# Kernel tuning notes

Hardware: AMD Instinct MI355X
Metric: run time of the kernel (lower is better)

The kernel has to match this reference:

```python
import jax, jax.numpy as jnp
import numpy as np

N = 50000       # node_num
E_RND = 1600000 # random edges (avg degree 32)
IN = 256        # in_dim
OUT = 128       # out_dim
NB = 10000      # queried nodes batch
SLOPE = 0.1     # leaky_relu slope_ratio


def setup_inputs() -> dict:
    key = jax.random.key(0)
    k = jax.random.split(key, 6)
    feats = jax.random.normal(k[0], (N, IN), dtype=jnp.float32)
    W = jax.random.normal(k[1], (OUT, IN), dtype=jnp.float32) * 0.05
    b = jax.random.normal(k[2], (OUT,), dtype=jnp.float32) * 0.05
    a = jax.random.normal(k[3], (2 * OUT,), dtype=jnp.float32) * 0.05
    rnd = jax.random.randint(k[4], (E_RND, 2), 0, N)
    loops = jnp.stack([jnp.arange(N), jnp.arange(N)], axis=1)  # self-loops, as in torch code
    edges = jnp.concatenate([rnd, loops], axis=0).astype(jnp.int32)  # [E,2] = (dst, src)
    node_idx = jax.random.randint(k[5], (NB,), 0, N).astype(jnp.int32)
    return dict(feats=feats, W=W, b=b, a=a, edges=edges, node_idx=node_idx)


def reference(feats, W, b, a, edges, node_idx):
    n = feats.shape[0]
    emb = feats @ W.T + b                      # [N, OUT]  (out_linear_layer)
    out_dim = emb.shape[1]
    # concat(emb[dst], emb[src]) @ a  ==  (emb @ a1)[dst] + (emb @ a2)[src]
    s_dst = emb @ a[:out_dim]                  # [N]
    s_src = emb @ a[out_dim:]                  # [N]
    dst, src = edges[:, 0], edges[:, 1]
    score = jnp.exp(jax.nn.leaky_relu(s_dst[dst] + s_src[src], negative_slope=SLOPE))  # [E]
    # sparse.mm(matrix, emb) and sparse.mm(matrix, ones) as segment sums over dst
    num = jax.ops.segment_sum(score[:, None] * emb[src], dst, num_segments=n)  # [N, OUT]
    den = jax.ops.segment_sum(score, dst, num_segments=n)                       # [N]
    out = num / den[:, None]
    return out[node_idx]
```

## Files before the change

### kernel.cpp

```cpp
#include <hip/hip_runtime.h>

#define IN_DIM 256
#define OUT_DIM 128
#define SLOPE 0.1f
#define CAP 128

typedef short bf16x8 __attribute__((ext_vector_type(8)));
typedef float f32x4  __attribute__((ext_vector_type(4)));

__device__ __forceinline__ unsigned short f2bf(float f) {
    unsigned u = __builtin_bit_cast(unsigned, f);
    return (unsigned short)((u + 0x7FFFu + ((u >> 16) & 1u)) >> 16);
}

__global__ __launch_bounds__(256) void gemm_mfma_kernel(
    const float* __restrict__ feats, const float* __restrict__ W,
    const float* __restrict__ bias, const float* __restrict__ a,
    unsigned short* __restrict__ emb_bf, float* __restrict__ s_dst,
    float* __restrict__ s_src, int* __restrict__ needed,
    int* __restrict__ cur, int n)
{
    __shared__ __align__(16) unsigned short A_s[128 * 128];
    __shared__ __align__(16) unsigned short W_s[128 * 128];
    __shared__ float sd_l[2][128];
    __shared__ float ss_l[2][128];

    const int t    = threadIdx.x;
    const int lane = t & 63;
    const int wid  = t >> 6;
    const int wr   = wid >> 1;
    const int wc   = wid & 1;
    const int row0 = blockIdx.x * 128;

    if (t < 128) {
        const int ci = row0 + t;
        if (ci < n) { needed[ci] = 0; cur[ci] = 0; }
    }

    const f32x4 z4 = {0.f, 0.f, 0.f, 0.f};
    f32x4 acc[4][4];
    #pragma unroll
    for (int mi = 0; mi < 4; ++mi)
        #pragma unroll
        for (int ni = 0; ni < 4; ++ni) acc[mi][ni] = z4;

    for (int ph = 0; ph < 2; ++ph) {
        const int k0 = ph * 128;
        if (ph) __syncthreads();

        #pragma unroll
        for (int i = 0; i < 8; ++i) {
            const int g = i * 256 + t;
            const int r = g >> 4;
            const int c = g & 15;
            const int gr = row0 + r;
            float4 v0 = make_float4(0.f,0.f,0.f,0.f), v1 = v0;
            if (gr < n) {
                v0 = *(const float4*)&feats[(size_t)gr * IN_DIM + k0 + c * 8];
                v1 = *(const float4*)&feats[(size_t)gr * IN_DIM + k0 + c * 8 + 4];
            }
            bf16x8 pk;
            pk[0]=(short)f2bf(v0.x); pk[1]=(short)f2bf(v0.y);
            pk[2]=(short)f2bf(v0.z); pk[3]=(short)f2bf(v0.w);
            pk[4]=(short)f2bf(v1.x); pk[5]=(short)f2bf(v1.y);
            pk[6]=(short)f2bf(v1.z); pk[7]=(short)f2bf(v1.w);
            const int off = (r * 128 + c * 8) ^ ((r & 7) << 3);
            *(bf16x8*)&A_s[off] = pk;
        }
        #pragma unroll
        for (int i = 0; i < 8; ++i) {
            const int g = i * 256 + t;
            const int r = g >> 4;
            const int c = g & 15;
            const float4 v0 = *(const float4*)&W[(size_t)r * IN_DIM + k0 + c * 8];
            const float4 v1 = *(const float4*)&W[(size_t)r * IN_DIM + k0 + c * 8 + 4];
            bf16x8 pk;
            pk[0]=(short)f2bf(v0.x); pk[1]=(short)f2bf(v0.y);
            pk[2]=(short)f2bf(v0.z); pk[3]=(short)f2bf(v0.w);
            pk[4]=(short)f2bf(v1.x); pk[5]=(short)f2bf(v1.y);
            pk[6]=(short)f2bf(v1.z); pk[7]=(short)f2bf(v1.w);
            const int off = (r * 128 + c * 8) ^ ((r & 7) << 3);
            *(bf16x8*)&W_s[off] = pk;
        }
        __syncthreads();

        #pragma unroll
        for (int ks = 0; ks < 4; ++ks) {
            const int kf = ks * 32 + (lane >> 4) * 8;
            bf16x8 af[4], wf[4];
            #pragma unroll
            for (int mi = 0; mi < 4; ++mi) {
                const int row = wr * 64 + mi * 16 + (lane & 15);
                const int off = (row * 128 + kf) ^ ((row & 7) << 3);
                af[mi] = *(const bf16x8*)&A_s[off];
            }
            #pragma unroll
            for (int ni = 0; ni < 4; ++ni) {
                const int col = wc * 64 + ni * 16 + (lane & 15);
                const int off = (col * 128 + kf) ^ ((col & 7) << 3);
                wf[ni] = *(const bf16x8*)&W_s[off];
            }
            #pragma unroll
            for (int mi = 0; mi < 4; ++mi)
                #pragma unroll
                for (int ni = 0; ni < 4; ++ni)
                    acc[mi][ni] = __builtin_amdgcn_mfma_f32_16x16x32_bf16(
                        af[mi], wf[ni], acc[mi][ni], 0, 0, 0);
        }
    }

    float bcol[4], avd[4], avs[4];
    #pragma unroll
    for (int ni = 0; ni < 4; ++ni) {
        const int col = wc * 64 + ni * 16 + (lane & 15);
        bcol[ni] = bias[col];
        avd[ni]  = a[col];
        avs[ni]  = a[OUT_DIM + col];
    }

    #pragma unroll
    for (int mi = 0; mi < 4; ++mi) {
        #pragma unroll
        for (int j = 0; j < 4; ++j) {
            const int rib = wr * 64 + mi * 16 + (lane >> 4) * 4 + j;
            const int row = row0 + rib;
            float pd = 0.f, ps = 0.f;
            if (row < n) {
                #pragma unroll
                for (int ni = 0; ni < 4; ++ni) {
                    const float v = acc[mi][ni][j] + bcol[ni];
                    emb_bf[(size_t)row * OUT_DIM + wc * 64 + ni * 16 + (lane & 15)] = f2bf(v);
                    pd = fmaf(v, avd[ni], pd);
                    ps = fmaf(v, avs[ni], ps);
                }
            }
            pd += __shfl_xor(pd, 1); ps += __shfl_xor(ps, 1);
            pd += __shfl_xor(pd, 2); ps += __shfl_xor(ps, 2);
            pd += __shfl_xor(pd, 4); ps += __shfl_xor(ps, 4);
            pd += __shfl_xor(pd, 8); ps += __shfl_xor(ps, 8);
            if ((lane & 15) == 0) { sd_l[wc][rib] = pd; ss_l[wc][rib] = ps; }
        }
    }
    __syncthreads();
    if (t < 128) {
        const int row = row0 + t;
        if (row < n) {
            s_dst[row] = sd_l[0][t] + sd_l[1][t];
            s_src[row] = ss_l[0][t] + ss_l[1][t];
        }
    }
}

__global__ void flag_kernel(const int* __restrict__ node_idx,
                            int* __restrict__ needed, int nb)
{
    const int i = blockIdx.x * blockDim.x + threadIdx.x;
    if (i < nb) needed[node_idx[i]] = 1;
}

__global__ __launch_bounds__(256) void scatter_kernel(
    const int* __restrict__ edges, const int* __restrict__ needed,
    int* __restrict__ cur, const float* __restrict__ s_dst,
    const float* __restrict__ s_src, int2* __restrict__ ew, int E)
{
    const int e = blockIdx.x * blockDim.x + threadIdx.x;
    if (e >= E) return;
    const int2 ed = reinterpret_cast<const int2*>(edges)[e];
    if (needed[ed.x]) {
        const float x = s_dst[ed.x] + s_src[ed.y];
        const float w = __expf(x >= 0.f ? x : SLOPE * x);
        const int p = atomicAdd(&cur[ed.x], 1);
        if (p < CAP)
            ew[(size_t)ed.x * CAP + p] = make_int2(ed.y, __float_as_int(w));
    }
}

__global__ __launch_bounds__(256) void agg_out_kernel(
    const int* __restrict__ node_idx, const int* __restrict__ cur,
    const int2* __restrict__ ew, const unsigned short* __restrict__ emb_bf,
    float* __restrict__ out, int nb)
{
    const int w    = (int)((blockIdx.x * blockDim.x + threadIdx.x) >> 6);
    const int lane = threadIdx.x & 63;
    if (w >= nb) return;

    const int dst = node_idx[w];
    int m = cur[dst];
    if (m > CAP) m = CAP;
    const int2* __restrict__ bucket = ew + (size_t)dst * CAP;

    float accx = 0.f, accy = 0.f, den = 0.f;

    for (int base = 0; base < m; base += 64) {
        const int rem = min(64, m - base);
        int   src = 0;
        float wt  = 0.f;
        if (lane < rem) {
            const int2 q = bucket[base + lane];
            src = q.x;
            wt  = __int_as_float(q.y);
        }
        int i = 0;
        for (; i + 4 <= rem; i += 4) {
            const int   s0 = __shfl(src, i),     s1 = __shfl(src, i + 1);
            const int   s2 = __shfl(src, i + 2), s3 = __shfl(src, i + 3);
            const float w0 = __shfl(wt, i),      w1 = __shfl(wt, i + 1);
            const float w2 = __shfl(wt, i + 2),  w3 = __shfl(wt, i + 3);
            const unsigned b0 = *(const unsigned*)&emb_bf[(size_t)s0 * OUT_DIM + 2 * lane];
            const unsigned b1 = *(const unsigned*)&emb_bf[(size_t)s1 * OUT_DIM + 2 * lane];
            const unsigned b2 = *(const unsigned*)&emb_bf[(size_t)s2 * OUT_DIM + 2 * lane];
            const unsigned b3 = *(const unsigned*)&emb_bf[(size_t)s3 * OUT_DIM + 2 * lane];
            den += (w0 + w1) + (w2 + w3);
            accx = fmaf(w0, __int_as_float((int)(b0 << 16)), accx);
            accy = fmaf(w0, __int_as_float((int)(b0 & 0xFFFF0000u)), accy);
            accx = fmaf(w1, __int_as_float((int)(b1 << 16)), accx);
            accy = fmaf(w1, __int_as_float((int)(b1 & 0xFFFF0000u)), accy);
            accx = fmaf(w2, __int_as_float((int)(b2 << 16)), accx);
            accy = fmaf(w2, __int_as_float((int)(b2 & 0xFFFF0000u)), accy);
            accx = fmaf(w3, __int_as_float((int)(b3 << 16)), accx);
            accy = fmaf(w3, __int_as_float((int)(b3 & 0xFFFF0000u)), accy);
        }
        for (; i < rem; ++i) {
            const int   s0 = __shfl(src, i);
            const float w0 = __shfl(wt, i);
            const unsigned b0 = *(const unsigned*)&emb_bf[(size_t)s0 * OUT_DIM + 2 * lane];
            den += w0;
            accx = fmaf(w0, __int_as_float((int)(b0 << 16)), accx);
            accy = fmaf(w0, __int_as_float((int)(b0 & 0xFFFF0000u)), accy);
        }
    }

    const float inv = 1.0f / den;
    float2 o; o.x = accx * inv; o.y = accy * inv;
    *reinterpret_cast<float2*>(&out[(size_t)w * OUT_DIM + 2 * lane]) = o;
}

extern "C" void kernel_launch(void* const* d_in, const int* in_sizes, int n_in,
                              void* d_out, int out_size, void* d_ws, size_t ws_size,
                              hipStream_t stream)
{
    const float* feats    = (const float*)d_in[0];
    const float* W        = (const float*)d_in[1];
    const float* bias     = (const float*)d_in[2];
    const float* a        = (const float*)d_in[3];
    const int*   edges    = (const int*)d_in[4];
    const int*   node_idx = (const int*)d_in[5];
    float*       out      = (float*)d_out;

    const int n  = in_sizes[0] / IN_DIM;
    const int E  = in_sizes[4] / 2;
    const int nb = in_sizes[5];

    char* ws = (char*)d_ws;
    unsigned short* emb_bf = (unsigned short*)ws;
    ws += (size_t)n * OUT_DIM * sizeof(unsigned short);
    float* s_dst = (float*)ws;  ws += (size_t)(n + 4) * sizeof(float);
    float* s_src = (float*)ws;  ws += (size_t)(n + 4) * sizeof(float);
    int*   needed= (int*)ws;    ws += (size_t)(n + 4) * sizeof(int);
    int*   cur   = (int*)ws;    ws += (size_t)(n + 4) * sizeof(int);
    int2*  ew    = (int2*)ws;   ws += (size_t)n * CAP * sizeof(int2);

    gemm_mfma_kernel<<<(n + 127) / 128, 256, 0, stream>>>(
        feats, W, bias, a, emb_bf, s_dst, s_src, needed, cur, n);
    flag_kernel     <<<(nb + 255) / 256, 256, 0, stream>>>(node_idx, needed, nb);
    scatter_kernel  <<<(E + 255) / 256, 256, 0, stream>>>(edges, needed, cur, s_dst, s_src, ew, E);
    agg_out_kernel  <<<(nb + 3) / 4, 256, 0, stream>>>(node_idx, cur, ew, emb_bf, out, nb);
}
```

Baseline: 63.52 us.

## Shrink GEMM row tile, stage emb stores through LDS, drop needed-node filter

The GEMM now handles 64 rows per block instead of 128, which halves the accumulator registers and launches twice as many blocks. The bf16 embedding is first written into padded shared memory and then stored to global memory as coalesced 16-byte vectors. The flag kernel and the `needed` array are removed, so the scatter pass now scores and buckets every edge, not only edges into queried nodes. That saves one launch and one memset-like write, but it raises scatter work, atomics and bucket writes roughly fivefold.

```diff
diff --git a/kernel.cpp b/kernel.cpp
--- a/kernel.cpp
+++ b/kernel.cpp
@@ -17,30 +17,29 @@
     const float* __restrict__ feats, const float* __restrict__ W,
     const float* __restrict__ bias, const float* __restrict__ a,
     unsigned short* __restrict__ emb_bf, float* __restrict__ s_dst,
-    float* __restrict__ s_src, int* __restrict__ needed,
-    int* __restrict__ cur, int n)
-{
-    __shared__ __align__(16) unsigned short A_s[128 * 128];
+    float* __restrict__ s_src, int* __restrict__ cur, int n)
+{
+    __shared__ __align__(16) unsigned short A_s[64 * 136];
     __shared__ __align__(16) unsigned short W_s[128 * 128];
-    __shared__ float sd_l[2][128];
-    __shared__ float ss_l[2][128];
+    __shared__ float sd_l[2][64];
+    __shared__ float ss_l[2][64];
 
     const int t    = threadIdx.x;
     const int lane = t & 63;
     const int wid  = t >> 6;
     const int wr   = wid >> 1;
     const int wc   = wid & 1;
-    const int row0 = blockIdx.x * 128;
-
-    if (t < 128) {
+    const int row0 = blockIdx.x * 64;
+
+    if (t < 64) {
         const int ci = row0 + t;
-        if (ci < n) { needed[ci] = 0; cur[ci] = 0; }
+        if (ci < n) cur[ci] = 0;
     }
 
     const f32x4 z4 = {0.f, 0.f, 0.f, 0.f};
-    f32x4 acc[4][4];
-    #pragma unroll
-    for (int mi = 0; mi < 4; ++mi)
+    f32x4 acc[2][4];
+    #pragma unroll
+    for (int mi = 0; mi < 2; ++mi)
         #pragma unroll
         for (int ni = 0; ni < 4; ++ni) acc[mi][ni] = z4;
 
@@ -49,7 +48,7 @@
         if (ph) __syncthreads();
 
         #pragma unroll
-        for (int i = 0; i < 8; ++i) {
+        for (int i = 0; i < 4; ++i) {
             const int g = i * 256 + t;
             const int r = g >> 4;
             const int c = g & 15;
@@ -87,10 +86,10 @@
         #pragma unroll
         for (int ks = 0; ks < 4; ++ks) {
             const int kf = ks * 32 + (lane >> 4) * 8;
-            bf16x8 af[4], wf[4];
-            #pragma unroll
-            for (int mi = 0; mi < 4; ++mi) {
-                const int row = wr * 64 + mi * 16 + (lane & 15);
+            bf16x8 af[2], wf[4];
+            #pragma unroll
+            for (int mi = 0; mi < 2; ++mi) {
+                const int row = wr * 32 + mi * 16 + (lane & 15);
                 const int off = (row * 128 + kf) ^ ((row & 7) << 3);
                 af[mi] = *(const bf16x8*)&A_s[off];
             }
@@ -101,7 +100,7 @@
                 wf[ni] = *(const bf16x8*)&W_s[off];
             }
             #pragma unroll
-            for (int mi = 0; mi < 4; ++mi)
+            for (int mi = 0; mi < 2; ++mi)
                 #pragma unroll
                 for (int ni = 0; ni < 4; ++ni)
                     acc[mi][ni] = __builtin_amdgcn_mfma_f32_16x16x32_bf16(
@@ -118,21 +117,20 @@
         avs[ni]  = a[OUT_DIM + col];
     }
 
-    #pragma unroll
-    for (int mi = 0; mi < 4; ++mi) {
+    __syncthreads();
+
+    #pragma unroll
+    for (int mi = 0; mi < 2; ++mi) {
         #pragma unroll
         for (int j = 0; j < 4; ++j) {
-            const int rib = wr * 64 + mi * 16 + (lane >> 4) * 4 + j;
-            const int row = row0 + rib;
+            const int rib = wr * 32 + mi * 16 + (lane >> 4) * 4 + j;
             float pd = 0.f, ps = 0.f;
-            if (row < n) {
-                #pragma unroll
-                for (int ni = 0; ni < 4; ++ni) {
-                    const float v = acc[mi][ni][j] + bcol[ni];
-                    emb_bf[(size_t)row * OUT_DIM + wc * 64 + ni * 16 + (lane & 15)] = f2bf(v);
-                    pd = fmaf(v, avd[ni], pd);
-                    ps = fmaf(v, avs[ni], ps);
-                }
+            #pragma unroll
+            for (int ni = 0; ni < 4; ++ni) {
+                const float v = acc[mi][ni][j] + bcol[ni];
+                A_s[rib * 136 + wc * 64 + ni * 16 + (lane & 15)] = f2bf(v);
+                pd = fmaf(v, avd[ni], pd);
+                ps = fmaf(v, avs[ni], ps);
             }
             pd += __shfl_xor(pd, 1); ps += __shfl_xor(ps, 1);
             pd += __shfl_xor(pd, 2); ps += __shfl_xor(ps, 2);
@@ -142,7 +140,19 @@
         }
     }
     __syncthreads();
-    if (t < 128) {
+
+    #pragma unroll
+    for (int i = 0; i < 4; ++i) {
+        const int g = i * 256 + t;
+        const int r = g >> 4;
+        const int c8 = g & 15;
+        const int gr = row0 + r;
+        if (gr < n) {
+            const bf16x8 v = *(const bf16x8*)&A_s[r * 136 + c8 * 8];
+            *(bf16x8*)&emb_bf[(size_t)gr * OUT_DIM + c8 * 8] = v;
+        }
+    }
+    if (t < 64) {
         const int row = row0 + t;
         if (row < n) {
             s_dst[row] = sd_l[0][t] + sd_l[1][t];
@@ -151,28 +161,19 @@
     }
 }
 
-__global__ void flag_kernel(const int* __restrict__ node_idx,
-                            int* __restrict__ needed, int nb)
-{
-    const int i = blockIdx.x * blockDim.x + threadIdx.x;
-    if (i < nb) needed[node_idx[i]] = 1;
-}
-
 __global__ __launch_bounds__(256) void scatter_kernel(
-    const int* __restrict__ edges, const int* __restrict__ needed,
-    int* __restrict__ cur, const float* __restrict__ s_dst,
-    const float* __restrict__ s_src, int2* __restrict__ ew, int E)
+    const int* __restrict__ edges, int* __restrict__ cur,
+    const float* __restrict__ s_dst, const float* __restrict__ s_src,
+    int2* __restrict__ ew, int E)
 {
     const int e = blockIdx.x * blockDim.x + threadIdx.x;
     if (e >= E) return;
     const int2 ed = reinterpret_cast<const int2*>(edges)[e];
-    if (needed[ed.x]) {
-        const float x = s_dst[ed.x] + s_src[ed.y];
-        const float w = __expf(x >= 0.f ? x : SLOPE * x);
-        const int p = atomicAdd(&cur[ed.x], 1);
-        if (p < CAP)
-            ew[(size_t)ed.x * CAP + p] = make_int2(ed.y, __float_as_int(w));
-    }
+    const float x = s_dst[ed.x] + s_src[ed.y];
+    const float w = __expf(x >= 0.f ? x : SLOPE * x);
+    const int p = atomicAdd(&cur[ed.x], 1);
+    if (p < CAP)
+        ew[(size_t)ed.x * CAP + p] = make_int2(ed.y, __float_as_int(w));
 }
 
 __global__ __launch_bounds__(256) void agg_out_kernel(
@@ -256,13 +257,11 @@
     ws += (size_t)n * OUT_DIM * sizeof(unsigned short);
     float* s_dst = (float*)ws;  ws += (size_t)(n + 4) * sizeof(float);
     float* s_src = (float*)ws;  ws += (size_t)(n + 4) * sizeof(float);
-    int*   needed= (int*)ws;    ws += (size_t)(n + 4) * sizeof(int);
     int*   cur   = (int*)ws;    ws += (size_t)(n + 4) * sizeof(int);
     int2*  ew    = (int2*)ws;   ws += (size_t)n * CAP * sizeof(int2);
 
-    gemm_mfma_kernel<<<(n + 127) / 128, 256, 0, stream>>>(
-        feats, W, bias, a, emb_bf, s_dst, s_src, needed, cur, n);
-    flag_kernel     <<<(nb + 255) / 256, 256, 0, stream>>>(node_idx, needed, nb);
-    scatter_kernel  <<<(E + 255) / 256, 256, 0, stream>>>(edges, needed, cur, s_dst, s_src, ew, E);
+    gemm_mfma_kernel<<<(n + 63) / 64, 256, 0, stream>>>(
+        feats, W, bias, a, emb_bf, s_dst, s_src, cur, n);
+    scatter_kernel  <<<(E + 255) / 256, 256, 0, stream>>>(edges, cur, s_dst, s_src, ew, E);
     agg_out_kernel  <<<(nb + 3) / 4, 256, 0, stream>>>(node_idx, cur, ew, emb_bf, out, nb);
 }
```

Result: slower. 130.5 us (+105.4%).

## Pre-convert inputs to bf16 and stage GEMM tiles via direct global-to-LDS loads

Applied to the files above, without the earlier changes.

Adds a separate conversion kernel that turns feats and W into bf16 buffers in the workspace. The GEMM then fills its LDS tiles with global_load_lds 16-byte direct copies, with the XOR swizzle applied on the source side, instead of loading fp32, converting in registers and writing to LDS. The goal is to cut register and VALU work and LDS write traffic in the GEMM staging. The cost is an extra full pass over feats (read fp32, write bf16, read bf16 again) plus one more kernel launch. The padded rows of the bf16 buffer are never written by the conversion kernel, so the last tile reads uninitialized data for rows beyond n.

```diff
diff --git a/kernel.cpp b/kernel.cpp
--- a/kernel.cpp
+++ b/kernel.cpp
@@ -7,14 +7,39 @@
 
 typedef short bf16x8 __attribute__((ext_vector_type(8)));
 typedef float f32x4  __attribute__((ext_vector_type(4)));
+typedef unsigned short ushort4v __attribute__((ext_vector_type(4)));
 
 __device__ __forceinline__ unsigned short f2bf(float f) {
     unsigned u = __builtin_bit_cast(unsigned, f);
     return (unsigned short)((u + 0x7FFFu + ((u >> 16) & 1u)) >> 16);
 }
 
+__device__ __forceinline__ void gld_lds16(const void* g, void* l) {
+    __builtin_amdgcn_global_load_lds(
+        (const __attribute__((address_space(1))) void*)g,
+        (__attribute__((address_space(3))) void*)l, 16, 0, 0);
+}
+
+__global__ __launch_bounds__(256) void cvt_kernel(
+    const float* __restrict__ feats, const float* __restrict__ W,
+    unsigned short* __restrict__ fb, unsigned short* __restrict__ wb,
+    int nf4, int nw4)
+{
+    const int stride = gridDim.x * blockDim.x;
+    const int total = nf4 + nw4;
+    for (int i = blockIdx.x * blockDim.x + threadIdx.x; i < total; i += stride) {
+        float4 v;
+        if (i < nf4) v = reinterpret_cast<const float4*>(feats)[i];
+        else         v = reinterpret_cast<const float4*>(W)[i - nf4];
+        ushort4v o;
+        o[0] = f2bf(v.x); o[1] = f2bf(v.y); o[2] = f2bf(v.z); o[3] = f2bf(v.w);
+        if (i < nf4) *reinterpret_cast<ushort4v*>(&fb[4 * (size_t)i]) = o;
+        else         *reinterpret_cast<ushort4v*>(&wb[4 * (size_t)(i - nf4)]) = o;
+    }
+}
+
 __global__ __launch_bounds__(256) void gemm_mfma_kernel(
-    const float* __restrict__ feats, const float* __restrict__ W,
+    const unsigned short* __restrict__ fb, const unsigned short* __restrict__ wb,
     const float* __restrict__ bias, const float* __restrict__ a,
     unsigned short* __restrict__ emb_bf, float* __restrict__ s_dst,
     float* __restrict__ s_src, int* __restrict__ needed,
@@ -37,6 +62,9 @@
         if (ci < n) { needed[ci] = 0; cur[ci] = 0; }
     }
 
+    const int rlo = lane >> 4;
+    const int cA  = lane & 15;
+
     const f32x4 z4 = {0.f, 0.f, 0.f, 0.f};
     f32x4 acc[4][4];
     #pragma unroll
@@ -49,38 +77,14 @@
         if (ph) __syncthreads();
 
         #pragma unroll
-        for (int i = 0; i < 8; ++i) {
-            const int g = i * 256 + t;
-            const int r = g >> 4;
-            const int c = g & 15;
-            const int gr = row0 + r;
-            float4 v0 = make_float4(0.f,0.f,0.f,0.f), v1 = v0;
-            if (gr < n) {
-                v0 = *(const float4*)&feats[(size_t)gr * IN_DIM + k0 + c * 8];
-                v1 = *(const float4*)&feats[(size_t)gr * IN_DIM + k0 + c * 8 + 4];
-            }
-            bf16x8 pk;
-            pk[0]=(short)f2bf(v0.x); pk[1]=(short)f2bf(v0.y);
-            pk[2]=(short)f2bf(v0.z); pk[3]=(short)f2bf(v0.w);
-            pk[4]=(short)f2bf(v1.x); pk[5]=(short)f2bf(v1.y);
-            pk[6]=(short)f2bf(v1.z); pk[7]=(short)f2bf(v1.w);
-            const int off = (r * 128 + c * 8) ^ ((r & 7) << 3);
-            *(bf16x8*)&A_s[off] = pk;
-        }
-        #pragma unroll
-        for (int i = 0; i < 8; ++i) {
-            const int g = i * 256 + t;
-            const int r = g >> 4;
-            const int c = g & 15;
-            const float4 v0 = *(const float4*)&W[(size_t)r * IN_DIM + k0 + c * 8];
-            const float4 v1 = *(const float4*)&W[(size_t)r * IN_DIM + k0 + c * 8 + 4];
-            bf16x8 pk;
-            pk[0]=(short)f2bf(v0.x); pk[1]=(short)f2bf(v0.y);
-            pk[2]=(short)f2bf(v0.z); pk[3]=(short)f2bf(v0.w);
-            pk[4]=(short)f2bf(v1.x); pk[5]=(short)f2bf(v1.y);
-            pk[6]=(short)f2bf(v1.z); pk[7]=(short)f2bf(v1.w);
-            const int off = (r * 128 + c * 8) ^ ((r & 7) << 3);
-            *(bf16x8*)&W_s[off] = pk;
+        for (int j = 0; j < 8; ++j) {
+            const int slot = wid * 8 + j;
+            const int r    = slot * 4 + rlo;
+            const int ch   = cA ^ (r & 7);
+            gld_lds16(fb + (size_t)(row0 + r) * IN_DIM + k0 + (ch << 3),
+                      &A_s[slot * 512]);
+            gld_lds16(wb + (size_t)r * IN_DIM + k0 + (ch << 3),
+                      &W_s[slot * 512]);
         }
         __syncthreads();
 
@@ -250,18 +254,27 @@
     const int n  = in_sizes[0] / IN_DIM;
     const int E  = in_sizes[4] / 2;
     const int nb = in_sizes[5];
+    const int npad = ((n + 127) / 128) * 128;
 
     char* ws = (char*)d_ws;
     unsigned short* emb_bf = (unsigned short*)ws;
     ws += (size_t)n * OUT_DIM * sizeof(unsigned short);
+    unsigned short* fb = (unsigned short*)ws;
+    ws += (size_t)npad * IN_DIM * sizeof(unsigned short);
+    unsigned short* wb = (unsigned short*)ws;
+    ws += (size_t)OUT_DIM * IN_DIM * sizeof(unsigned short);
     float* s_dst = (float*)ws;  ws += (size_t)(n + 4) * sizeof(float);
     float* s_src = (float*)ws;  ws += (size_t)(n + 4) * sizeof(float);
     int*   needed= (int*)ws;    ws += (size_t)(n + 4) * sizeof(int);
     int*   cur   = (int*)ws;    ws += (size_t)(n + 4) * sizeof(int);
     int2*  ew    = (int2*)ws;   ws += (size_t)n * CAP * sizeof(int2);
 
-    gemm_mfma_kernel<<<(n + 127) / 128, 256, 0, stream>>>(
-        feats, W, bias, a, emb_bf, s_dst, s_src, needed, cur, n);
+    const int nf4 = n * IN_DIM / 4;
+    const int nw4 = OUT_DIM * IN_DIM / 4;
+
+    cvt_kernel      <<<2048, 256, 0, stream>>>(feats, W, fb, wb, nf4, nw4);
+    gemm_mfma_kernel<<<npad / 128, 256, 0, stream>>>(
+        fb, wb, bias, a, emb_bf, s_dst, s_src, needed, cur, n);
     flag_kernel     <<<(nb + 255) / 256, 256, 0, stream>>>(node_idx, needed, nb);
     scatter_kernel  <<<(E + 255) / 256, 256, 0, stream>>>(edges, needed, cur, s_dst, s_src, ew, E);
     agg_out_kernel  <<<(nb + 3) / 4, 256, 0, stream>>>(node_idx, cur, ew, emb_bf, out, nb);
```

Measured after the change: 69.12 us. +8.8%, slower.

## Restructure GEMM as persistent per-wave row chunks with full W in LDS

Applied to the files above, without the earlier changes.

The GEMM kernel now runs a fixed grid of 512 blocks. Each block loads the whole 128x256 weight matrix into LDS once as bf16. Each wave then loops over 16-row chunks, reading feature rows straight from global memory into MFMA registers, and computes all 128 output columns itself. This removes the A-tile LDS staging, the block-level syncs between K phases and the cross-wave shared reduction of attention scores. In exchange, every block re-reads the full W, the 64KB LDS footprint limits occupancy, and the fixed grid size assumes enough threads to zero the needed/cur arrays.

```diff
diff --git a/kernel.cpp b/kernel.cpp
--- a/kernel.cpp
+++ b/kernel.cpp
@@ -11,6 +11,13 @@
 __device__ __forceinline__ unsigned short f2bf(float f) {
     unsigned u = __builtin_bit_cast(unsigned, f);
     return (unsigned short)((u + 0x7FFFu + ((u >> 16) & 1u)) >> 16);
+}
+
+__device__ __forceinline__ void pack8(const float4& v0, const float4& v1, bf16x8& pk) {
+    pk[0]=(short)f2bf(v0.x); pk[1]=(short)f2bf(v0.y);
+    pk[2]=(short)f2bf(v0.z); pk[3]=(short)f2bf(v0.w);
+    pk[4]=(short)f2bf(v1.x); pk[5]=(short)f2bf(v1.y);
+    pk[6]=(short)f2bf(v1.z); pk[7]=(short)f2bf(v1.w);
 }
 
 __global__ __launch_bounds__(256) void gemm_mfma_kernel(
@@ -18,135 +25,99 @@
     const float* __restrict__ bias, const float* __restrict__ a,
     unsigned short* __restrict__ emb_bf, float* __restrict__ s_dst,
     float* __restrict__ s_src, int* __restrict__ needed,
-    int* __restrict__ cur, int n)
-{
-    __shared__ __align__(16) unsigned short A_s[128 * 128];
-    __shared__ __align__(16) unsigned short W_s[128 * 128];
-    __shared__ float sd_l[2][128];
-    __shared__ float ss_l[2][128];
+    int* __restrict__ cur, int n, int nchunks)
+{
+    __shared__ __align__(16) unsigned short W_s[128 * 256];
 
     const int t    = threadIdx.x;
     const int lane = t & 63;
     const int wid  = t >> 6;
-    const int wr   = wid >> 1;
-    const int wc   = wid & 1;
-    const int row0 = blockIdx.x * 128;
-
-    if (t < 128) {
-        const int ci = row0 + t;
-        if (ci < n) { needed[ci] = 0; cur[ci] = 0; }
-    }
-
-    const f32x4 z4 = {0.f, 0.f, 0.f, 0.f};
-    f32x4 acc[4][4];
+
+    const int gi = blockIdx.x * 256 + t;
+    if (gi < n) { needed[gi] = 0; cur[gi] = 0; }
+
     #pragma unroll
-    for (int mi = 0; mi < 4; ++mi)
-        #pragma unroll
-        for (int ni = 0; ni < 4; ++ni) acc[mi][ni] = z4;
-
-    for (int ph = 0; ph < 2; ++ph) {
-        const int k0 = ph * 128;
-        if (ph) __syncthreads();
-
-        #pragma unroll
-        for (int i = 0; i < 8; ++i) {
-            const int g = i * 256 + t;
-            const int r = g >> 4;
-            const int c = g & 15;
-            const int gr = row0 + r;
-            float4 v0 = make_float4(0.f,0.f,0.f,0.f), v1 = v0;
-            if (gr < n) {
-                v0 = *(const float4*)&feats[(size_t)gr * IN_DIM + k0 + c * 8];
-                v1 = *(const float4*)&feats[(size_t)gr * IN_DIM + k0 + c * 8 + 4];
-            }
-            bf16x8 pk;
-            pk[0]=(short)f2bf(v0.x); pk[1]=(short)f2bf(v0.y);
-            pk[2]=(short)f2bf(v0.z); pk[3]=(short)f2bf(v0.w);
-            pk[4]=(short)f2bf(v1.x); pk[5]=(short)f2bf(v1.y);
-            pk[6]=(short)f2bf(v1.z); pk[7]=(short)f2bf(v1.w);
-            const int off = (r * 128 + c * 8) ^ ((r & 7) << 3);
-            *(bf16x8*)&A_s[off] = pk;
-        }
-        #pragma unroll
-        for (int i = 0; i < 8; ++i) {
-            const int g = i * 256 + t;
-            const int r = g >> 4;
-            const int c = g & 15;
-            const float4 v0 = *(const float4*)&W[(size_t)r * IN_DIM + k0 + c * 8];
-            const float4 v1 = *(const float4*)&W[(size_t)r * IN_DIM + k0 + c * 8 + 4];
-            bf16x8 pk;
-            pk[0]=(short)f2bf(v0.x); pk[1]=(short)f2bf(v0.y);
-            pk[2]=(short)f2bf(v0.z); pk[3]=(short)f2bf(v0.w);
-            pk[4]=(short)f2bf(v1.x); pk[5]=(short)f2bf(v1.y);
-            pk[6]=(short)f2bf(v1.z); pk[7]=(short)f2bf(v1.w);
-            const int off = (r * 128 + c * 8) ^ ((r & 7) << 3);
-            *(bf16x8*)&W_s[off] = pk;
-        }
-        __syncthreads();
-
-        #pragma unroll
-        for (int ks = 0; ks < 4; ++ks) {
-            const int kf = ks * 32 + (lane >> 4) * 8;
-            bf16x8 af[4], wf[4];
-            #pragma unroll
-            for (int mi = 0; mi < 4; ++mi) {
-                const int row = wr * 64 + mi * 16 + (lane & 15);
-                const int off = (row * 128 + kf) ^ ((row & 7) << 3);
-                af[mi] = *(const bf16x8*)&A_s[off];
-            }
-            #pragma unroll
-            for (int ni = 0; ni < 4; ++ni) {
-                const int col = wc * 64 + ni * 16 + (lane & 15);
-                const int off = (col * 128 + kf) ^ ((col & 7) << 3);
-                wf[ni] = *(const bf16x8*)&W_s[off];
-            }
-            #pragma unroll
-            for (int mi = 0; mi < 4; ++mi)
-                #pragma unroll
-                for (int ni = 0; ni < 4; ++ni)
-                    acc[mi][ni] = __builtin_amdgcn_mfma_f32_16x16x32_bf16(
-                        af[mi], wf[ni], acc[mi][ni], 0, 0, 0);
-        }
-    }
-
-    float bcol[4], avd[4], avs[4];
+    for (int i = 0; i < 16; ++i) {
+        const int g = i * 256 + t;
+        const int r = g >> 5;
+        const int c = g & 31;
+        const float* p = &W[(size_t)r * IN_DIM + c * 8];
+        const float4 v0 = *(const float4*)p;
+        const float4 v1 = *(const float4*)(p + 4);
+        bf16x8 pk; pack8(v0, v1, pk);
+        *(bf16x8*)&W_s[r * 256 + ((c ^ (r & 7)) << 3)] = pk;
+    }
+    __syncthreads();
+
+    const int rl = lane & 15;
+    const int kq = lane >> 4;
+    float bcol[8], avd[8], avs[8];
     #pragma unroll
-    for (int ni = 0; ni < 4; ++ni) {
-        const int col = wc * 64 + ni * 16 + (lane & 15);
+    for (int ni = 0; ni < 8; ++ni) {
+        const int col = ni * 16 + rl;
         bcol[ni] = bias[col];
         avd[ni]  = a[col];
         avs[ni]  = a[OUT_DIM + col];
     }
 
-    #pragma unroll
-    for (int mi = 0; mi < 4; ++mi) {
+    const int wstart  = blockIdx.x * 4 + wid;
+    const int wstride = gridDim.x * 4;
+
+    for (int chunk = wstart; chunk < nchunks; chunk += wstride) {
+        const int row0 = chunk * 16;
+        const int arow = row0 + rl;
+        const int lrow = arow < n ? arow : n - 1;
+        const float* prow = &feats[(size_t)lrow * IN_DIM + kq * 8];
+
+        bf16x8 af[8];
+        #pragma unroll
+        for (int ks = 0; ks < 8; ++ks) {
+            const float4 v0 = *(const float4*)(prow + ks * 32);
+            const float4 v1 = *(const float4*)(prow + ks * 32 + 4);
+            pack8(v0, v1, af[ks]);
+        }
+
+        f32x4 acc[8];
+        #pragma unroll
+        for (int ni = 0; ni < 8; ++ni) acc[ni] = {0.f, 0.f, 0.f, 0.f};
+
+        #pragma unroll
+        for (int ks = 0; ks < 8; ++ks) {
+            const int kf = ks * 32 + kq * 8;
+            #pragma unroll
+            for (int ni = 0; ni < 8; ++ni) {
+                const int col = ni * 16 + rl;
+                const int off = (col * 256 + kf) ^ ((col & 7) << 3);
+                const bf16x8 wf = *(const bf16x8*)&W_s[off];
+                acc[ni] = __builtin_amdgcn_mfma_f32_16x16x32_bf16(
+                    af[ks], wf, acc[ni], 0, 0, 0);
+            }
+        }
+
+        float pd[4] = {0.f,0.f,0.f,0.f}, ps[4] = {0.f,0.f,0.f,0.f};
+        #pragma unroll
+        for (int ni = 0; ni < 8; ++ni) {
+            #pragma unroll
+            for (int j = 0; j < 4; ++j) {
+                const float v = acc[ni][j] + bcol[ni];
+                const int row = row0 + kq * 4 + j;
+                if (row < n)
+                    emb_bf[(size_t)row * OUT_DIM + ni * 16 + rl] = f2bf(v);
+                pd[j] = fmaf(v, avd[ni], pd[j]);
+                ps[j] = fmaf(v, avs[ni], ps[j]);
+            }
+        }
         #pragma unroll
         for (int j = 0; j < 4; ++j) {
-            const int rib = wr * 64 + mi * 16 + (lane >> 4) * 4 + j;
-            const int row = row0 + rib;
-            float pd = 0.f, ps = 0.f;
-            if (row < n) {
-                #pragma unroll
-                for (int ni = 0; ni < 4; ++ni) {
-                    const float v = acc[mi][ni][j] + bcol[ni];
-                    emb_bf[(size_t)row * OUT_DIM + wc * 64 + ni * 16 + (lane & 15)] = f2bf(v);
-                    pd = fmaf(v, avd[ni], pd);
-                    ps = fmaf(v, avs[ni], ps);
-                }
+            pd[j] += __shfl_xor(pd[j], 1); ps[j] += __shfl_xor(ps[j], 1);
+            pd[j] += __shfl_xor(pd[j], 2); ps[j] += __shfl_xor(ps[j], 2);
+            pd[j] += __shfl_xor(pd[j], 4); ps[j] += __shfl_xor(ps[j], 4);
+            pd[j] += __shfl_xor(pd[j], 8); ps[j] += __shfl_xor(ps[j], 8);
+            const int row = row0 + kq * 4 + j;
+            if (rl == 0 && row < n) {
+                s_dst[row] = pd[j];
+                s_src[row] = ps[j];
             }
-            pd += __shfl_xor(pd, 1); ps += __shfl_xor(ps, 1);
-            pd += __shfl_xor(pd, 2); ps += __shfl_xor(ps, 2);
-            pd += __shfl_xor(pd, 4); ps += __shfl_xor(ps, 4);
-            pd += __shfl_xor(pd, 8); ps += __shfl_xor(ps, 8);
-            if ((lane & 15) == 0) { sd_l[wc][rib] = pd; ss_l[wc][rib] = ps; }
-        }
-    }
-    __syncthreads();
-    if (t < 128) {
-        const int row = row0 + t;
-        if (row < n) {
-            s_dst[row] = sd_l[0][t] + sd_l[1][t];
-            s_src[row] = ss_l[0][t] + ss_l[1][t];
         }
     }
 }
@@ -250,6 +221,7 @@
     const int n  = in_sizes[0] / IN_DIM;
     const int E  = in_sizes[4] / 2;
     const int nb = in_sizes[5];
+    const int nchunks = (n + 15) / 16;
 
     char* ws = (char*)d_ws;
     unsigned short* emb_bf = (unsigned short*)ws;
@@ -260,8 +232,8 @@
     int*   cur   = (int*)ws;    ws += (size_t)(n + 4) * sizeof(int);
     int2*  ew    = (int2*)ws;   ws += (size_t)n * CAP * sizeof(int2);
 
-    gemm_mfma_kernel<<<(n + 127) / 128, 256, 0, stream>>>(
-        feats, W, bias, a, emb_bf, s_dst, s_src, needed, cur, n);
+    gemm_mfma_kernel<<<512, 256, 0, stream>>>(
+        feats, W, bias, a, emb_bf, s_dst, s_src, needed, cur, n, nchunks);
     flag_kernel     <<<(nb + 255) / 256, 256, 0, stream>>>(node_idx, needed, nb);
     scatter_kernel  <<<(E + 255) / 256, 256, 0, stream>>>(edges, needed, cur, s_dst, s_src, ew, E);
     agg_out_kernel  <<<(nb + 3) / 4, 256, 0, stream>>>(node_idx, cur, ew, emb_bf, out, nb);
```

After: 76.21 us. +20.0%, slower.
